# Optimization experiments

Measured on AMD Instinct MI355X. Metric: run time of the kernel, lower is better.

## Reference

```python
import jax, jax.numpy as jnp
import numpy as np
import math

SQRT7 = math.sqrt(7.0)
EPS = 1e-05


def int4_quant(x):
    # absmean scaling to [-8, 7]; out = x_q * (beta*sqrt7) / sqrt7
    beta = jnp.mean(jnp.abs(x), axis=-1, keepdims=True)
    x_q = jnp.clip(jnp.round(x * SQRT7 / (beta + EPS)), -8, 7)
    return x_q * (beta * SQRT7) / SQRT7


def int8_quant(x):
    # absmax scaling to [-128, 127]
    gamma = jnp.max(jnp.abs(x), axis=-1, keepdims=True)
    x_q = jnp.clip(jnp.round(x * 127.0 / (gamma + EPS)), -128, 127)
    return x_q * gamma / 127.0


def bitlinear(x, w, scale):
    # ternary (1.58-bit) weight fake-quant: round(W / mean|W|) clamped to {-1,0,1}
    w_mean = jnp.mean(jnp.abs(w))
    w_q = jnp.clip(jnp.round(w / (w_mean + EPS)), -1.0, 1.0)
    w_eff = w_q * w_mean * scale  # [out, in]
    return jnp.einsum('...i,oi->...o', x, w_eff)


def setup_inputs() -> dict:
    key = jax.random.key(0)
    ks = jax.random.split(key, 4)
    H, I = 4096, 11008
    B, S = 2, 2048
    # kaiming_uniform(a=sqrt(5)) -> bound = 1/sqrt(fan_in)
    x = jax.random.normal(ks[0], (B, S, H), dtype=jnp.float32)
    w_gate = jax.random.uniform(ks[1], (I, H), jnp.float32, -1.0, 1.0) / np.sqrt(H)
    w_up = jax.random.uniform(ks[2], (I, H), jnp.float32, -1.0, 1.0) / np.sqrt(H)
    w_down = jax.random.uniform(ks[3], (H, I), jnp.float32, -1.0, 1.0) / np.sqrt(I)
    ones = jnp.ones((1,), jnp.float32)
    return {"x": x, "w_gate": w_gate, "w_up": w_up, "w_down": w_down,
            "s_gate": ones, "s_up": ones, "s_down": ones}


def reference(x, w_gate, w_up, w_down, s_gate, s_up, s_down):
    xq = int4_quant(x)                          # [B,S,H]
    gate = bitlinear(xq, w_gate, s_gate)        # [B,S,I]
    up = bitlinear(xq, w_up, s_up)              # [B,S,I]
    gate = jnp.square(jax.nn.relu(gate))        # ReLU^2 gate
    inter = int8_quant(up * gate)               # [B,S,I]
    return bitlinear(inter, w_down, s_down)     # [B,S,H]
```

## Files before the change

### kernel.cpp

```cpp
#include <hip/hip_runtime.h>
#include <stdint.h>


typedef int i32x4 __attribute__((ext_vector_type(4)));
typedef short s16x8 __attribute__((ext_vector_type(8)));

#define HD 4096
#define ID 11008
#define MD 4096
#define WN 45088768
#define N1 22016
#define QEPS 1e-5f
#define SQRT7 2.6457513110645907f

#define MFMA_I8(a, b, c) __builtin_amdgcn_mfma_i32_16x16x64_i8(a, b, c, 0, 0, 0)

__device__ __forceinline__ void gload_lds16(const char* g, char* l) {
  __builtin_amdgcn_global_load_lds((const __attribute__((address_space(1))) void*)g,
                                   (__attribute__((address_space(3))) void*)l, 16, 0, 0);
}

__device__ __forceinline__ void stage64(const char* __restrict__ g, int ldk,
                                        char* lds, int w, int l) {
  int t = w * 64 + l;
  int r = t >> 2, sl = (t & 3) ^ ((t >> 3) & 3);
  const char* gp = g + (size_t)r * ldk + (sl << 4);
  char* lp = lds + w * 1024;
#pragma unroll
  for (int i = 0; i < 2; ++i) {
    gload_lds16(gp, lp);
    gp += (size_t)128 * ldk;
    lp += 8192;
  }
}

__device__ __forceinline__ void gemm_core(const char* __restrict__ ga,
                                          const char* __restrict__ gb,
                                          int ldk, int nt, char* lds,
                                          i32x4 (&acc)[8][4], int w, int l) {
  const int wr = (w >> 2) * 128, wc = (w & 3) * 64;
  const int lr = l & 15;
  const int sw4 = (((l >> 4) ^ ((l >> 1) & 3)) << 4);
#pragma unroll
  for (int pt = 0; pt < 3; ++pt) {
    stage64(ga + (size_t)pt * 64, ldk, lds + pt * 32768, w, l);
    stage64(gb + (size_t)pt * 64, ldk, lds + pt * 32768 + 16384, w, l);
  }
  for (int t = 0; t < nt; ++t) {
    if (t + 2 < nt)      asm volatile("s_waitcnt vmcnt(8)" ::: "memory");
    else if (t + 1 < nt) asm volatile("s_waitcnt vmcnt(4)" ::: "memory");
    else                 asm volatile("s_waitcnt vmcnt(0)" ::: "memory");
    __builtin_amdgcn_s_barrier();
    if (t + 3 < nt) {
      char* buf = lds + ((t + 3) & 3) * 32768;
      stage64(ga + (size_t)(t + 3) * 64, ldk, buf, w, l);
      stage64(gb + (size_t)(t + 3) * 64, ldk, buf + 16384, w, l);
    }
    const char* Ab = lds + (t & 3) * 32768;
    const char* Bb = Ab + 16384;
    i32x4 af[8], bf[4];
#pragma unroll
    for (int mi = 0; mi < 8; ++mi)
      af[mi] = *(const i32x4*)(Ab + (wr + mi * 16 + lr) * 64 + sw4);
#pragma unroll
    for (int ni = 0; ni < 4; ++ni)
      bf[ni] = *(const i32x4*)(Bb + (wc + ni * 16 + lr) * 64 + sw4);
    __builtin_amdgcn_s_setprio(1);
#pragma unroll
    for (int ni = 0; ni < 4; ++ni)
#pragma unroll
      for (int mi = 0; mi < 8; ++mi)
        acc[mi][ni] = MFMA_I8(af[mi], bf[ni], acc[mi][ni]);
    __builtin_amdgcn_s_setprio(0);
  }
}

__global__ __launch_bounds__(512, 2) void gemm1_kernel(
    const char* __restrict__ A, const char* __restrict__ B, short* __restrict__ C) {
  __shared__ __align__(16) char lds[131072];
  int t = threadIdx.x, w = t >> 6, l = t & 63;
  int wgid = ((int)blockIdx.x & 7) * 172 + ((int)blockIdx.x >> 3);
  int bm = wgid & 15, bn = wgid >> 4;
  i32x4 acc[8][4] = {};
  gemm_core(A + (size_t)bm * 256 * HD, B + (size_t)bn * 256 * HD, HD, HD / 64,
            lds, acc, w, l);
  int wr = (w >> 2) * 128, wc = (w & 3) * 64, lr = l & 15, lj = (l >> 4) * 4;
#pragma unroll
  for (int mi = 0; mi < 8; ++mi) {
    int row = bm * 256 + wr + mi * 16 + lj;
#pragma unroll
    for (int ni = 0; ni < 4; ++ni) {
      int col = bn * 256 + wc + ni * 16 + lr;
#pragma unroll
      for (int j = 0; j < 4; ++j) {
        int v = acc[mi][ni][j];
        v = v < -32768 ? -32768 : (v > 32767 ? 32767 : v);
        C[(size_t)(row + j) * N1 + col] = (short)v;
      }
    }
  }
}

__global__ __launch_bounds__(512, 2) void gemm_down_kernel(
    const char* __restrict__ A, const char* __restrict__ B, float* __restrict__ out,
    const float* __restrict__ gammaF, const double* __restrict__ sums,
    const float* __restrict__ sd) {
  __shared__ __align__(16) char lds[131072];
  int t = threadIdx.x, w = t >> 6, l = t & 63;
  int wgid = ((int)blockIdx.x & 7) * 32 + ((int)blockIdx.x >> 3);
  int bm = wgid & 15, bn = wgid >> 4;
  i32x4 acc[8][4] = {};
  gemm_core(A + (size_t)bm * 256 * ID, B + (size_t)bn * 256 * ID, ID, ID / 64,
            lds, acc, w, l);
  float wdm = (float)(sums[2] * (1.0 / (double)WN)) * sd[0] * (1.f / 127.f);
  int wr = (w >> 2) * 128, wc = (w & 3) * 64, lr = l & 15, lj = (l >> 4) * 4;
#pragma unroll
  for (int mi = 0; mi < 8; ++mi) {
    int row = bm * 256 + wr + mi * 16 + lj;
    float sa[4];
#pragma unroll
    for (int j = 0; j < 4; ++j) sa[j] = gammaF[row + j] * wdm;
#pragma unroll
    for (int ni = 0; ni < 4; ++ni) {
      int col = bn * 256 + wc + ni * 16 + lr;
#pragma unroll
      for (int j = 0; j < 4; ++j)
        out[(size_t)(row + j) * HD + col] = (float)acc[mi][ni][j] * sa[j];
    }
  }
}

__device__ __forceinline__ int pack4div(float4 v, float mul, float den, float lo, float hi) {
  int a = (int)fminf(fmaxf(rintf((v.x * mul) / den), lo), hi);
  int b = (int)fminf(fmaxf(rintf((v.y * mul) / den), lo), hi);
  int c = (int)fminf(fmaxf(rintf((v.z * mul) / den), lo), hi);
  int d = (int)fminf(fmaxf(rintf((v.w * mul) / den), lo), hi);
  return (a & 255) | ((b & 255) << 8) | ((c & 255) << 16) | ((d & 255) << 24);
}

__global__ __launch_bounds__(256) void abssum_kernel(const float4* __restrict__ w,
                                                     int n8, double* __restrict__ out) {
  float s = 0.f;
  int stride = gridDim.x * blockDim.x;
  for (int i = blockIdx.x * blockDim.x + threadIdx.x; i < n8; i += stride) {
    float4 v0 = w[i * 2], v1 = w[i * 2 + 1];
    s += fabsf(v0.x) + fabsf(v0.y) + fabsf(v0.z) + fabsf(v0.w);
    s += fabsf(v1.x) + fabsf(v1.y) + fabsf(v1.z) + fabsf(v1.w);
  }
#pragma unroll
  for (int off = 32; off > 0; off >>= 1) s += __shfl_down(s, off);
  __shared__ float red[4];
  int l = threadIdx.x & 63, wv = threadIdx.x >> 6;
  if (l == 0) red[wv] = s;
  __syncthreads();
  if (threadIdx.x == 0) {
    double tt = (double)red[0] + (double)red[1] + (double)red[2] + (double)red[3];
    atomicAdd(out, tt);
  }
}

__global__ __launch_bounds__(256) void quantx_kernel(const float* __restrict__ x,
                                                     char* __restrict__ xq,
                                                     float* __restrict__ scale_x) {
  int row = blockIdx.x;
  const float4* xr = (const float4*)(x + (size_t)row * HD);
  int t = threadIdx.x;
  float4 v[4];
  float s = 0.f;
#pragma unroll
  for (int k = 0; k < 4; ++k) {
    v[k] = xr[t + k * 256];
    s += fabsf(v[k].x) + fabsf(v[k].y) + fabsf(v[k].z) + fabsf(v[k].w);
  }
#pragma unroll
  for (int off = 32; off > 0; off >>= 1) s += __shfl_down(s, off);
  __shared__ float red[4];
  int l = t & 63, wv = t >> 6;
  if (l == 0) red[wv] = s;
  __syncthreads();
  float beta = (red[0] + red[1] + red[2] + red[3]) * (1.f / (float)HD);
  if (t == 0) scale_x[row] = (beta * SQRT7) / SQRT7;
  float den = beta + QEPS;
  int* qr = (int*)(xq + (size_t)row * HD);
#pragma unroll
  for (int k = 0; k < 4; ++k)
    qr[t + k * 256] = pack4div(v[k], SQRT7, den, -8.f, 7.f);
}

__global__ __launch_bounds__(256) void quantw_kernel(const float4* __restrict__ w,
                                                     int4* __restrict__ wq,
                                                     const double* __restrict__ sum) {
  float mean = (float)(*sum * (1.0 / (double)WN));
  float den = mean + QEPS;
  int n16 = WN / 16;
  int stride = gridDim.x * blockDim.x;
  for (int i = blockIdx.x * blockDim.x + threadIdx.x; i < n16; i += stride) {
    float4 v0 = w[i * 4 + 0], v1 = w[i * 4 + 1], v2 = w[i * 4 + 2], v3 = w[i * 4 + 3];
    int4 o;
    o.x = pack4div(v0, 1.f, den, -1.f, 1.f);
    o.y = pack4div(v1, 1.f, den, -1.f, 1.f);
    o.z = pack4div(v2, 1.f, den, -1.f, 1.f);
    o.w = pack4div(v3, 1.f, den, -1.f, 1.f);
    wq[i] = o;
  }
}

__global__ __launch_bounds__(256) void combine_kernel(
    const short* __restrict__ C, const float* __restrict__ scale_x,
    const double* __restrict__ sums, const float* __restrict__ sg,
    const float* __restrict__ su, float* __restrict__ gammaF,
    char* __restrict__ hq) {
  int row = blockIdx.x, t = threadIdx.x;
  float gm = (float)(sums[0] * (1.0 / (double)WN)) * sg[0];
  float um = (float)(sums[1] * (1.0 / (double)WN)) * su[0];
  float sx = scale_x[row];
  float sxg = sx * gm, sxu = sx * um;
  const s16x8* g8 = (const s16x8*)(C + (size_t)row * N1);
  const s16x8* u8 = (const s16x8*)(C + (size_t)row * N1 + ID);
  float hv[6][8];
  float m = 0.f;
#pragma unroll
  for (int k = 0; k < 6; ++k) {
    int c = t + k * 256;
    if (c < ID / 8) {
      s16x8 gi = __builtin_nontemporal_load(&g8[c]);
      s16x8 ui = __builtin_nontemporal_load(&u8[c]);
#pragma unroll
      for (int e = 0; e < 8; ++e) {
        float rg = fmaxf((float)gi[e] * sxg, 0.f);
        hv[k][e] = ((float)ui[e] * sxu) * (rg * rg);
        m = fmaxf(m, fabsf(hv[k][e]));
      }
    }
  }
#pragma unroll
  for (int off = 32; off > 0; off >>= 1) m = fmaxf(m, __shfl_xor(m, off));
  __shared__ float red[4];
  if ((t & 63) == 0) red[t >> 6] = m;
  __syncthreads();
  float gamma = fmaxf(fmaxf(red[0], red[1]), fmaxf(red[2], red[3]));
  if (t == 0) gammaF[row] = gamma;
  float den = gamma + QEPS;
  int2* hr = (int2*)(hq + (size_t)row * ID);
#pragma unroll
  for (int k = 0; k < 6; ++k) {
    int c = t + k * 256;
    if (c < ID / 8) {
      int2 o;
      o.x = pack4div(make_float4(hv[k][0], hv[k][1], hv[k][2], hv[k][3]), 127.f, den, -128.f, 127.f);
      o.y = pack4div(make_float4(hv[k][4], hv[k][5], hv[k][6], hv[k][7]), 127.f, den, -128.f, 127.f);
      hr[c] = o;
    }
  }
}

extern "C" void kernel_launch(void* const* d_in, const int* in_sizes, int n_in,
                              void* d_out, int out_size, void* d_ws, size_t ws_size,
                              hipStream_t stream) {
  (void)in_sizes; (void)n_in; (void)out_size; (void)ws_size;
  const float* x = (const float*)d_in[0];
  const float* w_gate = (const float*)d_in[1];
  const float* w_up = (const float*)d_in[2];
  const float* w_down = (const float*)d_in[3];
  const float* s_gate = (const float*)d_in[4];
  const float* s_up = (const float*)d_in[5];
  const float* s_down = (const float*)d_in[6];
  float* out = (float*)d_out;

  char* p = (char*)d_ws;
  double* sums = (double*)p;
  float* gammaF = (float*)(p + 256);
  float* scale_x = (float*)(p + 256 + 16384);
  char* xq = p + 33024;
  char* wgq = xq + 16777216UL;
  char* wuq = wgq + (size_t)WN;
  char* wdq = wuq + (size_t)WN;
  short* C16 = (short*)(wdq + (size_t)WN);
  char* hq = (char*)C16 + 180355072UL;

  (void)hipMemsetAsync(p, 0, 256, stream);

  abssum_kernel<<<2048, 256, 0, stream>>>((const float4*)w_gate, WN / 8, sums + 0);
  quantw_kernel<<<2048, 256, 0, stream>>>((const float4*)w_gate, (int4*)wgq, sums + 0);
  abssum_kernel<<<2048, 256, 0, stream>>>((const float4*)w_up, WN / 8, sums + 1);
  quantw_kernel<<<2048, 256, 0, stream>>>((const float4*)w_up, (int4*)wuq, sums + 1);
  abssum_kernel<<<2048, 256, 0, stream>>>((const float4*)w_down, WN / 8, sums + 2);
  quantw_kernel<<<2048, 256, 0, stream>>>((const float4*)w_down, (int4*)wdq, sums + 2);

  quantx_kernel<<<MD, 256, 0, stream>>>(x, xq, scale_x);

  gemm1_kernel<<<1376, 512, 0, stream>>>(xq, wgq, C16);

  combine_kernel<<<MD, 256, 0, stream>>>(C16, scale_x, sums, s_gate, s_up, gammaF, hq);

  gemm_down_kernel<<<256, 512, 0, stream>>>(hq, wdq, out, gammaF, sums, s_down);
}
```

Measured before the change: 850.3 us.

## Use 4 waves with 128x128 warp tiles and double-buffered fragment prefetch

```diff
diff --git a/kernel.cpp b/kernel.cpp
--- a/kernel.cpp
+++ b/kernel.cpp
@@ -20,76 +20,106 @@
                                    (__attribute__((address_space(3))) void*)l, 16, 0, 0);
 }
 
-__device__ __forceinline__ void stage64(const char* __restrict__ g, int ldk,
-                                        char* lds, int w, int l) {
-  int t = w * 64 + l;
+__device__ __forceinline__ void stage64q(const char* __restrict__ g, int ldk,
+                                         char* lds, int t) {
   int r = t >> 2, sl = (t & 3) ^ ((t >> 3) & 3);
   const char* gp = g + (size_t)r * ldk + (sl << 4);
-  char* lp = lds + w * 1024;
-#pragma unroll
-  for (int i = 0; i < 2; ++i) {
+  char* lp = lds + t * 16;
+#pragma unroll
+  for (int i = 0; i < 4; ++i) {
     gload_lds16(gp, lp);
-    gp += (size_t)128 * ldk;
-    lp += 8192;
-  }
+    gp += (size_t)64 * ldk;
+    lp += 4096;
+  }
+}
+
+__device__ __forceinline__ void read_frags(const char* __restrict__ slot,
+                                           int wr, int wc, int lr, int sw4,
+                                           i32x4 (&A)[8], i32x4 (&B)[8]) {
+  const char* Ab = slot;
+  const char* Bb = slot + 16384;
+#pragma unroll
+  for (int i = 0; i < 8; ++i)
+    A[i] = *(const i32x4*)(Ab + (wr + i * 16 + lr) * 64 + sw4);
+#pragma unroll
+  for (int i = 0; i < 8; ++i)
+    B[i] = *(const i32x4*)(Bb + (wc + i * 16 + lr) * 64 + sw4);
+}
+
+__device__ __forceinline__ void mfma_burst(const i32x4 (&A)[8], const i32x4 (&B)[8],
+                                           i32x4 (&acc)[8][8]) {
+  __builtin_amdgcn_s_setprio(1);
+#pragma unroll
+  for (int n = 0; n < 8; ++n)
+#pragma unroll
+    for (int m = 0; m < 8; ++m)
+      acc[m][n] = MFMA_I8(A[m], B[n], acc[m][n]);
+  __builtin_amdgcn_s_setprio(0);
 }
 
 __device__ __forceinline__ void gemm_core(const char* __restrict__ ga,
                                           const char* __restrict__ gb,
                                           int ldk, int nt, char* lds,
-                                          i32x4 (&acc)[8][4], int w, int l) {
-  const int wr = (w >> 2) * 128, wc = (w & 3) * 64;
+                                          i32x4 (&acc)[8][8], int w, int l) {
+  const int t256 = w * 64 + l;
+  const int wr = (w >> 1) * 128, wc = (w & 1) * 128;
   const int lr = l & 15;
   const int sw4 = (((l >> 4) ^ ((l >> 1) & 3)) << 4);
+  i32x4 A0[8], B0[8], A1[8], B1[8];
 #pragma unroll
   for (int pt = 0; pt < 3; ++pt) {
-    stage64(ga + (size_t)pt * 64, ldk, lds + pt * 32768, w, l);
-    stage64(gb + (size_t)pt * 64, ldk, lds + pt * 32768 + 16384, w, l);
-  }
-  for (int t = 0; t < nt; ++t) {
-    if (t + 2 < nt)      asm volatile("s_waitcnt vmcnt(8)" ::: "memory");
-    else if (t + 1 < nt) asm volatile("s_waitcnt vmcnt(4)" ::: "memory");
-    else                 asm volatile("s_waitcnt vmcnt(0)" ::: "memory");
-    __builtin_amdgcn_s_barrier();
-    if (t + 3 < nt) {
-      char* buf = lds + ((t + 3) & 3) * 32768;
-      stage64(ga + (size_t)(t + 3) * 64, ldk, buf, w, l);
-      stage64(gb + (size_t)(t + 3) * 64, ldk, buf + 16384, w, l);
-    }
-    const char* Ab = lds + (t & 3) * 32768;
-    const char* Bb = Ab + 16384;
-    i32x4 af[8], bf[4];
-#pragma unroll
-    for (int mi = 0; mi < 8; ++mi)
-      af[mi] = *(const i32x4*)(Ab + (wr + mi * 16 + lr) * 64 + sw4);
-#pragma unroll
-    for (int ni = 0; ni < 4; ++ni)
-      bf[ni] = *(const i32x4*)(Bb + (wc + ni * 16 + lr) * 64 + sw4);
-    __builtin_amdgcn_s_setprio(1);
-#pragma unroll
-    for (int ni = 0; ni < 4; ++ni)
-#pragma unroll
-      for (int mi = 0; mi < 8; ++mi)
-        acc[mi][ni] = MFMA_I8(af[mi], bf[ni], acc[mi][ni]);
-    __builtin_amdgcn_s_setprio(0);
-  }
-}
-
-__global__ __launch_bounds__(512, 2) void gemm1_kernel(
+    stage64q(ga + (size_t)pt * 64, ldk, lds + pt * 32768, t256);
+    stage64q(gb + (size_t)pt * 64, ldk, lds + pt * 32768 + 16384, t256);
+  }
+  asm volatile("s_waitcnt vmcnt(16)" ::: "memory");
+  __builtin_amdgcn_s_barrier();
+  read_frags(lds, wr, wc, lr, sw4, A0, B0);
+  for (int t = 0; t < nt; t += 2) {
+    {
+      if (t + 2 < nt) asm volatile("s_waitcnt vmcnt(8)" ::: "memory");
+      else            asm volatile("s_waitcnt vmcnt(0)" ::: "memory");
+      __builtin_amdgcn_s_barrier();
+      if (t + 3 < nt) {
+        char* buf = lds + ((t + 3) & 3) * 32768;
+        stage64q(ga + (size_t)(t + 3) * 64, ldk, buf, t256);
+        stage64q(gb + (size_t)(t + 3) * 64, ldk, buf + 16384, t256);
+      }
+      read_frags(lds + ((t + 1) & 3) * 32768, wr, wc, lr, sw4, A1, B1);
+      mfma_burst(A0, B0, acc);
+    }
+    {
+      int u = t + 1;
+      if (u + 1 < nt) {
+        if (u + 2 < nt) asm volatile("s_waitcnt vmcnt(8)" ::: "memory");
+        else            asm volatile("s_waitcnt vmcnt(0)" ::: "memory");
+        __builtin_amdgcn_s_barrier();
+        if (u + 3 < nt) {
+          char* buf = lds + ((u + 3) & 3) * 32768;
+          stage64q(ga + (size_t)(u + 3) * 64, ldk, buf, t256);
+          stage64q(gb + (size_t)(u + 3) * 64, ldk, buf + 16384, t256);
+        }
+        read_frags(lds + ((u + 1) & 3) * 32768, wr, wc, lr, sw4, A0, B0);
+      }
+      mfma_burst(A1, B1, acc);
+    }
+  }
+}
+
+__global__ __launch_bounds__(256, 1) void gemm1_kernel(
     const char* __restrict__ A, const char* __restrict__ B, short* __restrict__ C) {
   __shared__ __align__(16) char lds[131072];
   int t = threadIdx.x, w = t >> 6, l = t & 63;
   int wgid = ((int)blockIdx.x & 7) * 172 + ((int)blockIdx.x >> 3);
   int bm = wgid & 15, bn = wgid >> 4;
-  i32x4 acc[8][4] = {};
+  i32x4 acc[8][8] = {};
   gemm_core(A + (size_t)bm * 256 * HD, B + (size_t)bn * 256 * HD, HD, HD / 64,
             lds, acc, w, l);
-  int wr = (w >> 2) * 128, wc = (w & 3) * 64, lr = l & 15, lj = (l >> 4) * 4;
+  int wr = (w >> 1) * 128, wc = (w & 1) * 128, lr = l & 15, lj = (l >> 4) * 4;
 #pragma unroll
   for (int mi = 0; mi < 8; ++mi) {
     int row = bm * 256 + wr + mi * 16 + lj;
 #pragma unroll
-    for (int ni = 0; ni < 4; ++ni) {
+    for (int ni = 0; ni < 8; ++ni) {
       int col = bn * 256 + wc + ni * 16 + lr;
 #pragma unroll
       for (int j = 0; j < 4; ++j) {
@@ -101,7 +131,7 @@
   }
 }
 
-__global__ __launch_bounds__(512, 2) void gemm_down_kernel(
+__global__ __launch_bounds__(256, 1) void gemm_down_kernel(
     const char* __restrict__ A, const char* __restrict__ B, float* __restrict__ out,
     const float* __restrict__ gammaF, const double* __restrict__ sums,
     const float* __restrict__ sd) {
@@ -109,11 +139,11 @@
   int t = threadIdx.x, w = t >> 6, l = t & 63;
   int wgid = ((int)blockIdx.x & 7) * 32 + ((int)blockIdx.x >> 3);
   int bm = wgid & 15, bn = wgid >> 4;
-  i32x4 acc[8][4] = {};
+  i32x4 acc[8][8] = {};
   gemm_core(A + (size_t)bm * 256 * ID, B + (size_t)bn * 256 * ID, ID, ID / 64,
             lds, acc, w, l);
   float wdm = (float)(sums[2] * (1.0 / (double)WN)) * sd[0] * (1.f / 127.f);
-  int wr = (w >> 2) * 128, wc = (w & 3) * 64, lr = l & 15, lj = (l >> 4) * 4;
+  int wr = (w >> 1) * 128, wc = (w & 1) * 128, lr = l & 15, lj = (l >> 4) * 4;
 #pragma unroll
   for (int mi = 0; mi < 8; ++mi) {
     int row = bm * 256 + wr + mi * 16 + lj;
@@ -121,7 +151,7 @@
 #pragma unroll
     for (int j = 0; j < 4; ++j) sa[j] = gammaF[row + j] * wdm;
 #pragma unroll
-    for (int ni = 0; ni < 4; ++ni) {
+    for (int ni = 0; ni < 8; ++ni) {
       int col = bn * 256 + wc + ni * 16 + lr;
 #pragma unroll
       for (int j = 0; j < 4; ++j)
@@ -289,9 +319,9 @@
 
   quantx_kernel<<<MD, 256, 0, stream>>>(x, xq, scale_x);
 
-  gemm1_kernel<<<1376, 512, 0, stream>>>(xq, wgq, C16);
+  gemm1_kernel<<<1376, 256, 0, stream>>>(xq, wgq, C16);
 
   combine_kernel<<<MD, 256, 0, stream>>>(C16, scale_x, sums, s_gate, s_up, gammaF, hq);
 
-  gemm_down_kernel<<<256, 512, 0, stream>>>(hq, wdq, out, gammaF, sums, s_down);
-}
+  gemm_down_kernel<<<256, 256, 0, stream>>>(hq, wdq, out, gammaF, sums, s_down);
+}
```

New measurement: 1.994 ms. 134% more time.

## Load GEMM B operand directly into registers, halve LDS staging footprint

Applied to the files above, without the earlier changes.

```diff
diff --git a/kernel.cpp b/kernel.cpp
--- a/kernel.cpp
+++ b/kernel.cpp
@@ -20,64 +20,74 @@
                                    (__attribute__((address_space(3))) void*)l, 16, 0, 0);
 }
 
-__device__ __forceinline__ void stage64(const char* __restrict__ g, int ldk,
-                                        char* lds, int w, int l) {
-  int t = w * 64 + l;
-  int r = t >> 2, sl = (t & 3) ^ ((t >> 3) & 3);
+__device__ __forceinline__ void stageA(const char* __restrict__ g, int ldk,
+                                       char* lds, int t512) {
+  int r = t512 >> 2, sl = (t512 & 3) ^ ((t512 >> 3) & 3);
   const char* gp = g + (size_t)r * ldk + (sl << 4);
-  char* lp = lds + w * 1024;
-#pragma unroll
-  for (int i = 0; i < 2; ++i) {
-    gload_lds16(gp, lp);
-    gp += (size_t)128 * ldk;
-    lp += 8192;
-  }
+  gload_lds16(gp, lds + t512 * 16);
+  gload_lds16(gp + (size_t)128 * ldk, lds + t512 * 16 + 8192);
+}
+
+__device__ __forceinline__ void loadB(const char* __restrict__ gb, int ldk,
+                                      int tile, int wc, int lr, int khi,
+                                      i32x4 (&bq)[4]) {
+  const char* bp = gb + (size_t)tile * 64 + khi;
+#pragma unroll
+  for (int ni = 0; ni < 4; ++ni)
+    bq[ni] = *(const i32x4*)(bp + (size_t)(wc + ni * 16 + lr) * ldk);
+}
+
+__device__ __forceinline__ void gemm_iter(const char* __restrict__ ga,
+                                          const char* __restrict__ gb,
+                                          int ldk, int nt, char* lds, int t,
+                                          i32x4 (&bq)[4], i32x4 (&acc)[8][4],
+                                          int t512, int wr, int wc, int lr,
+                                          int sw4, int khi) {
+  if (t + 2 < nt)      asm volatile("s_waitcnt vmcnt(6)" ::: "memory");
+  else if (t + 1 < nt) asm volatile("s_waitcnt vmcnt(4)" ::: "memory");
+  else                 asm volatile("s_waitcnt vmcnt(0)" ::: "memory");
+  __builtin_amdgcn_s_barrier();
+  if (t + 3 < nt)
+    stageA(ga + (size_t)(t + 3) * 64, ldk, lds + ((t + 3) & 3) * 16384, t512);
+  const char* Ab = lds + (t & 3) * 16384;
+  i32x4 af[8];
+#pragma unroll
+  for (int mi = 0; mi < 8; ++mi)
+    af[mi] = *(const i32x4*)(Ab + (wr + mi * 16 + lr) * 64 + sw4);
+  __builtin_amdgcn_s_setprio(1);
+#pragma unroll
+  for (int ni = 0; ni < 4; ++ni)
+#pragma unroll
+    for (int mi = 0; mi < 8; ++mi)
+      acc[mi][ni] = MFMA_I8(af[mi], bq[ni], acc[mi][ni]);
+  __builtin_amdgcn_s_setprio(0);
+  if (t + 2 < nt)
+    loadB(gb, ldk, t + 2, wc, lr, khi, bq);
 }
 
 __device__ __forceinline__ void gemm_core(const char* __restrict__ ga,
                                           const char* __restrict__ gb,
                                           int ldk, int nt, char* lds,
                                           i32x4 (&acc)[8][4], int w, int l) {
+  const int t512 = w * 64 + l;
   const int wr = (w >> 2) * 128, wc = (w & 3) * 64;
-  const int lr = l & 15;
+  const int lr = l & 15, khi = (l >> 4) * 16;
   const int sw4 = (((l >> 4) ^ ((l >> 1) & 3)) << 4);
-#pragma unroll
-  for (int pt = 0; pt < 3; ++pt) {
-    stage64(ga + (size_t)pt * 64, ldk, lds + pt * 32768, w, l);
-    stage64(gb + (size_t)pt * 64, ldk, lds + pt * 32768 + 16384, w, l);
-  }
-  for (int t = 0; t < nt; ++t) {
-    if (t + 2 < nt)      asm volatile("s_waitcnt vmcnt(8)" ::: "memory");
-    else if (t + 1 < nt) asm volatile("s_waitcnt vmcnt(4)" ::: "memory");
-    else                 asm volatile("s_waitcnt vmcnt(0)" ::: "memory");
-    __builtin_amdgcn_s_barrier();
-    if (t + 3 < nt) {
-      char* buf = lds + ((t + 3) & 3) * 32768;
-      stage64(ga + (size_t)(t + 3) * 64, ldk, buf, w, l);
-      stage64(gb + (size_t)(t + 3) * 64, ldk, buf + 16384, w, l);
-    }
-    const char* Ab = lds + (t & 3) * 32768;
-    const char* Bb = Ab + 16384;
-    i32x4 af[8], bf[4];
-#pragma unroll
-    for (int mi = 0; mi < 8; ++mi)
-      af[mi] = *(const i32x4*)(Ab + (wr + mi * 16 + lr) * 64 + sw4);
-#pragma unroll
-    for (int ni = 0; ni < 4; ++ni)
-      bf[ni] = *(const i32x4*)(Bb + (wc + ni * 16 + lr) * 64 + sw4);
-    __builtin_amdgcn_s_setprio(1);
-#pragma unroll
-    for (int ni = 0; ni < 4; ++ni)
-#pragma unroll
-      for (int mi = 0; mi < 8; ++mi)
-        acc[mi][ni] = MFMA_I8(af[mi], bf[ni], acc[mi][ni]);
-    __builtin_amdgcn_s_setprio(0);
+  i32x4 bqE[4], bqO[4];
+  stageA(ga, ldk, lds, t512);
+  stageA(ga + 64, ldk, lds + 16384, t512);
+  loadB(gb, ldk, 0, wc, lr, khi, bqE);
+  stageA(ga + 128, ldk, lds + 32768, t512);
+  loadB(gb, ldk, 1, wc, lr, khi, bqO);
+  for (int t = 0; t < nt; t += 2) {
+    gemm_iter(ga, gb, ldk, nt, lds, t,     bqE, acc, t512, wr, wc, lr, sw4, khi);
+    gemm_iter(ga, gb, ldk, nt, lds, t + 1, bqO, acc, t512, wr, wc, lr, sw4, khi);
   }
 }
 
 __global__ __launch_bounds__(512, 2) void gemm1_kernel(
     const char* __restrict__ A, const char* __restrict__ B, short* __restrict__ C) {
-  __shared__ __align__(16) char lds[131072];
+  __shared__ __align__(16) char lds[65536];
   int t = threadIdx.x, w = t >> 6, l = t & 63;
   int wgid = ((int)blockIdx.x & 7) * 172 + ((int)blockIdx.x >> 3);
   int bm = wgid & 15, bn = wgid >> 4;
@@ -105,7 +115,7 @@
     const char* __restrict__ A, const char* __restrict__ B, float* __restrict__ out,
     const float* __restrict__ gammaF, const double* __restrict__ sums,
     const float* __restrict__ sd) {
-  __shared__ __align__(16) char lds[131072];
+  __shared__ __align__(16) char lds[65536];
   int t = threadIdx.x, w = t >> 6, l = t & 63;
   int wgid = ((int)blockIdx.x & 7) * 32 + ((int)blockIdx.x >> 3);
   int bm = wgid & 15, bn = wgid >> 4;
```

Result: slower. 1.171 ms (+37.7%).

## Shrink GEMM tiles to 256x128 with 4 waves and a triple-buffered LDS ring

Applied to the files above, without the earlier changes.

```diff
diff --git a/kernel.cpp b/kernel.cpp
--- a/kernel.cpp
+++ b/kernel.cpp
@@ -12,25 +12,33 @@
 #define N1 22016
 #define QEPS 1e-5f
 #define SQRT7 2.6457513110645907f
-
-#define MFMA_I8(a, b, c) __builtin_amdgcn_mfma_i32_16x16x64_i8(a, b, c, 0, 0, 0)
+#define SLOT 24576
+
+__device__ __forceinline__ void mfma_a(i32x4& acc, i32x4 a, i32x4 b) {
+  asm("v_mfma_i32_16x16x64_i8 %0, %1, %2, %0" : "+a"(acc) : "v"(a), "v"(b));
+}
 
 __device__ __forceinline__ void gload_lds16(const char* g, char* l) {
   __builtin_amdgcn_global_load_lds((const __attribute__((address_space(1))) void*)g,
                                    (__attribute__((address_space(3))) void*)l, 16, 0, 0);
 }
 
-__device__ __forceinline__ void stage64(const char* __restrict__ g, int ldk,
-                                        char* lds, int w, int l) {
-  int t = w * 64 + l;
-  int r = t >> 2, sl = (t & 3) ^ ((t >> 3) & 3);
-  const char* gp = g + (size_t)r * ldk + (sl << 4);
-  char* lp = lds + w * 1024;
+__device__ __forceinline__ void stageA3(const char* __restrict__ g, int ldk,
+                                        char* lds, int t256) {
+#pragma unroll
+  for (int i = 0; i < 4; ++i) {
+    int u = t256 + i * 256;
+    int r = u >> 2, sl = (u & 3) ^ ((u >> 3) & 3);
+    gload_lds16(g + (size_t)r * ldk + (sl << 4), lds + u * 16);
+  }
+}
+__device__ __forceinline__ void stageB3(const char* __restrict__ g, int ldk,
+                                        char* lds, int t256) {
 #pragma unroll
   for (int i = 0; i < 2; ++i) {
-    gload_lds16(gp, lp);
-    gp += (size_t)128 * ldk;
-    lp += 8192;
+    int u = t256 + i * 256;
+    int r = u >> 2, sl = (u & 3) ^ ((u >> 3) & 3);
+    gload_lds16(g + (size_t)r * ldk + (sl << 4), lds + u * 16);
   }
 }
 
@@ -38,59 +46,61 @@
                                           const char* __restrict__ gb,
                                           int ldk, int nt, char* lds,
                                           i32x4 (&acc)[8][4], int w, int l) {
-  const int wr = (w >> 2) * 128, wc = (w & 3) * 64;
+  const int t256 = w * 64 + l;
+  const int wr = (w >> 1) * 128, wc = (w & 1) * 64;
   const int lr = l & 15;
   const int sw4 = (((l >> 4) ^ ((l >> 1) & 3)) << 4);
-#pragma unroll
-  for (int pt = 0; pt < 3; ++pt) {
-    stage64(ga + (size_t)pt * 64, ldk, lds + pt * 32768, w, l);
-    stage64(gb + (size_t)pt * 64, ldk, lds + pt * 32768 + 16384, w, l);
-  }
+  stageA3(ga, ldk, lds, t256);
+  stageB3(gb, ldk, lds + 16384, t256);
+  stageA3(ga + 64, ldk, lds + SLOT, t256);
+  stageB3(gb + 64, ldk, lds + SLOT + 16384, t256);
+  int cur = 0;
   for (int t = 0; t < nt; ++t) {
-    if (t + 2 < nt)      asm volatile("s_waitcnt vmcnt(8)" ::: "memory");
-    else if (t + 1 < nt) asm volatile("s_waitcnt vmcnt(4)" ::: "memory");
-    else                 asm volatile("s_waitcnt vmcnt(0)" ::: "memory");
+    if (t + 1 < nt) asm volatile("s_waitcnt vmcnt(6)" ::: "memory");
+    else            asm volatile("s_waitcnt vmcnt(0)" ::: "memory");
     __builtin_amdgcn_s_barrier();
-    if (t + 3 < nt) {
-      char* buf = lds + ((t + 3) & 3) * 32768;
-      stage64(ga + (size_t)(t + 3) * 64, ldk, buf, w, l);
-      stage64(gb + (size_t)(t + 3) * 64, ldk, buf + 16384, w, l);
-    }
-    const char* Ab = lds + (t & 3) * 32768;
+    int pres = cur + 2; if (pres >= 3) pres -= 3;
+    if (t + 2 < nt) {
+      char* pre = lds + pres * SLOT;
+      stageA3(ga + (size_t)(t + 2) * 64, ldk, pre, t256);
+      stageB3(gb + (size_t)(t + 2) * 64, ldk, pre + 16384, t256);
+    }
+    const char* Ab = lds + cur * SLOT;
     const char* Bb = Ab + 16384;
     i32x4 af[8], bf[4];
 #pragma unroll
-    for (int mi = 0; mi < 8; ++mi)
-      af[mi] = *(const i32x4*)(Ab + (wr + mi * 16 + lr) * 64 + sw4);
-#pragma unroll
-    for (int ni = 0; ni < 4; ++ni)
-      bf[ni] = *(const i32x4*)(Bb + (wc + ni * 16 + lr) * 64 + sw4);
+    for (int i = 0; i < 8; ++i)
+      af[i] = *(const i32x4*)(Ab + (wr + i * 16 + lr) * 64 + sw4);
+#pragma unroll
+    for (int i = 0; i < 4; ++i)
+      bf[i] = *(const i32x4*)(Bb + (wc + i * 16 + lr) * 64 + sw4);
     __builtin_amdgcn_s_setprio(1);
 #pragma unroll
-    for (int ni = 0; ni < 4; ++ni)
-#pragma unroll
-      for (int mi = 0; mi < 8; ++mi)
-        acc[mi][ni] = MFMA_I8(af[mi], bf[ni], acc[mi][ni]);
+    for (int n = 0; n < 4; ++n)
+#pragma unroll
+      for (int m = 0; m < 8; ++m)
+        mfma_a(acc[m][n], af[m], bf[n]);
     __builtin_amdgcn_s_setprio(0);
-  }
-}
-
-__global__ __launch_bounds__(512, 2) void gemm1_kernel(
+    cur += 1; if (cur >= 3) cur -= 3;
+  }
+}
+
+__global__ __launch_bounds__(256, 2) void gemm1_kernel(
     const char* __restrict__ A, const char* __restrict__ B, short* __restrict__ C) {
-  __shared__ __align__(16) char lds[131072];
+  __shared__ __align__(16) char lds[3 * SLOT];
   int t = threadIdx.x, w = t >> 6, l = t & 63;
-  int wgid = ((int)blockIdx.x & 7) * 172 + ((int)blockIdx.x >> 3);
+  int wgid = ((int)blockIdx.x & 7) * 344 + ((int)blockIdx.x >> 3);
   int bm = wgid & 15, bn = wgid >> 4;
   i32x4 acc[8][4] = {};
-  gemm_core(A + (size_t)bm * 256 * HD, B + (size_t)bn * 256 * HD, HD, HD / 64,
+  gemm_core(A + (size_t)bm * 256 * HD, B + (size_t)bn * 128 * HD, HD, HD / 64,
             lds, acc, w, l);
-  int wr = (w >> 2) * 128, wc = (w & 3) * 64, lr = l & 15, lj = (l >> 4) * 4;
+  int wr = (w >> 1) * 128, wc = (w & 1) * 64, lr = l & 15, lj = (l >> 4) * 4;
 #pragma unroll
   for (int mi = 0; mi < 8; ++mi) {
     int row = bm * 256 + wr + mi * 16 + lj;
 #pragma unroll
     for (int ni = 0; ni < 4; ++ni) {
-      int col = bn * 256 + wc + ni * 16 + lr;
+      int col = bn * 128 + wc + ni * 16 + lr;
 #pragma unroll
       for (int j = 0; j < 4; ++j) {
         int v = acc[mi][ni][j];
@@ -101,19 +111,19 @@
   }
 }
 
-__global__ __launch_bounds__(512, 2) void gemm_down_kernel(
+__global__ __launch_bounds__(256, 2) void gemm_down_kernel(
     const char* __restrict__ A, const char* __restrict__ B, float* __restrict__ out,
     const float* __restrict__ gammaF, const double* __restrict__ sums,
     const float* __restrict__ sd) {
-  __shared__ __align__(16) char lds[131072];
+  __shared__ __align__(16) char lds[3 * SLOT];
   int t = threadIdx.x, w = t >> 6, l = t & 63;
-  int wgid = ((int)blockIdx.x & 7) * 32 + ((int)blockIdx.x >> 3);
+  int wgid = ((int)blockIdx.x & 7) * 64 + ((int)blockIdx.x >> 3);
   int bm = wgid & 15, bn = wgid >> 4;
   i32x4 acc[8][4] = {};
-  gemm_core(A + (size_t)bm * 256 * ID, B + (size_t)bn * 256 * ID, ID, ID / 64,
+  gemm_core(A + (size_t)bm * 256 * ID, B + (size_t)bn * 128 * ID, ID, ID / 64,
             lds, acc, w, l);
   float wdm = (float)(sums[2] * (1.0 / (double)WN)) * sd[0] * (1.f / 127.f);
-  int wr = (w >> 2) * 128, wc = (w & 3) * 64, lr = l & 15, lj = (l >> 4) * 4;
+  int wr = (w >> 1) * 128, wc = (w & 1) * 64, lr = l & 15, lj = (l >> 4) * 4;
 #pragma unroll
   for (int mi = 0; mi < 8; ++mi) {
     int row = bm * 256 + wr + mi * 16 + lj;
@@ -122,7 +132,7 @@
     for (int j = 0; j < 4; ++j) sa[j] = gammaF[row + j] * wdm;
 #pragma unroll
     for (int ni = 0; ni < 4; ++ni) {
-      int col = bn * 256 + wc + ni * 16 + lr;
+      int col = bn * 128 + wc + ni * 16 + lr;
 #pragma unroll
       for (int j = 0; j < 4; ++j)
         out[(size_t)(row + j) * HD + col] = (float)acc[mi][ni][j] * sa[j];
@@ -289,9 +299,9 @@
 
   quantx_kernel<<<MD, 256, 0, stream>>>(x, xq, scale_x);
 
-  gemm1_kernel<<<1376, 512, 0, stream>>>(xq, wgq, C16);
+  gemm1_kernel<<<2752, 256, 0, stream>>>(xq, wgq, C16);
 
   combine_kernel<<<MD, 256, 0, stream>>>(C16, scale_x, sums, s_gate, s_up, gammaF, hq);
 
-  gemm_down_kernel<<<256, 512, 0, stream>>>(hq, wdq, out, gammaF, sums, s_down);
-}
+  gemm_down_kernel<<<512, 256, 0, stream>>>(hq, wdq, out, gammaF, sums, s_down);
+}
```

After: 921.2 us. +8.3%, slower.
